# Kernel tuning notes

Hardware: AMD Instinct MI355X
Metric: run time of the kernel (lower is better)

## Reference

```python
import jax, jax.numpy as jnp
import numpy as np

N = 50000      # nodes
E = 800000     # edges (avg degree 16)
D = 128        # in_dim
H = 128        # hidden_dim
C = 10         # num_classes
G = 128        # graphs in batch
NUM_LAYERS = 3


def setup_inputs() -> dict:
    key = jax.random.key(0)
    ks = jax.random.split(key, 32)
    inp = {
        'features': jax.random.normal(ks[0], (N, D), dtype=jnp.float32),
        'src': jax.random.randint(ks[1], (E,), 0, N, dtype=jnp.int32),
        'dst': jax.random.randint(ks[2], (E,), 0, N, dtype=jnp.int32),
        'graph_ids': jnp.sort(jax.random.randint(ks[3], (N,), 0, G, dtype=jnp.int32)),
        'eps': jnp.zeros((NUM_LAYERS,), dtype=jnp.float32),  # learn_eps=True, init 0
    }
    # GIN MLPs: layer i has linear1 [in,H], linear2 [H,H] (stored as [in,out])
    ki = 4
    for i in range(NUM_LAYERS):
        din = D if i == 0 else H
        inp[f'w1_{i}'] = jax.random.normal(ks[ki], (din, H), dtype=jnp.float32) * (1.0 / np.sqrt(din)); ki += 1
        inp[f'b1_{i}'] = jnp.zeros((H,), dtype=jnp.float32)
        inp[f'w2_{i}'] = jax.random.normal(ks[ki], (H, H), dtype=jnp.float32) * (1.0 / np.sqrt(H)); ki += 1
        inp[f'b2_{i}'] = jnp.zeros((H,), dtype=jnp.float32)
    inp['wc1'] = jax.random.normal(ks[ki], (H, H), dtype=jnp.float32) * (1.0 / np.sqrt(H)); ki += 1
    inp['bc1'] = jnp.zeros((H,), dtype=jnp.float32)
    inp['wc2'] = jax.random.normal(ks[ki], (H, C), dtype=jnp.float32) * (1.0 / np.sqrt(H)); ki += 1
    inp['bc2'] = jnp.zeros((C,), dtype=jnp.float32)
    return inp


def _mlp(x, w1, b1, w2, b2):
    return jax.nn.relu(x @ w1 + b1) @ w2 + b2


def reference(features, src, dst, graph_ids, eps,
              w1_0, b1_0, w2_0, b2_0,
              w1_1, b1_1, w2_1, b2_1,
              w1_2, b1_2, w2_2, b2_2,
              wc1, bc1, wc2, bc2):
    mlps = [(w1_0, b1_0, w2_0, b2_0), (w1_1, b1_1, w2_1, b2_1), (w1_2, b1_2, w2_2, b2_2)]
    h = features
    for i, (w1, b1, w2, b2) in enumerate(mlps):
        # GINConv: aggregate sum of in-neighbor features (gather src, segment-sum into dst)
        agg = jax.ops.segment_sum(h[src], dst, num_segments=N)
        h = (1.0 + eps[i]) * h + agg
        h = _mlp(h, w1, b1, w2, b2)
        h = jax.nn.relu(h)
    # SumPooling: nodes -> graphs
    hg = jax.ops.segment_sum(h, graph_ids, num_segments=G)  # [G, H]
    out = jax.nn.relu(hg @ wc1 + bc1) @ wc2 + bc2            # [G, C]
    return out
```

## Files before the change

kernel.cpp:

```cpp
#include <hip/hip_runtime.h>

#define NN 50000
#define EE 800000
#define HH 128
#define CC 10
#define GG 128
#define NBK 782
#define NCH 98
#define CHUNK 8192

typedef __attribute__((ext_vector_type(8))) short short8;
typedef __attribute__((ext_vector_type(4))) float f32x4;

__device__ __forceinline__ ushort f2b(float f) {
    union { float f; uint u; } x; x.f = f;
    uint u = x.u;
    uint r = (u + 0x7fffu + ((u >> 16) & 1u)) >> 16;
    return (ushort)r;
}
__device__ __forceinline__ float lo2f(uint v) {
    union { uint u; float f; } x; x.u = v << 16; return x.f;
}
__device__ __forceinline__ float hi2f(uint v) {
    union { uint u; float f; } x; x.u = v & 0xffff0000u; return x.f;
}


__global__ __launch_bounds__(256) void hist_kernel(const int* __restrict__ dst,
                                                   int* __restrict__ hist) {
    __shared__ int hc[NBK];
    const int c = blockIdx.x, t = threadIdx.x;
    for (int k = t; k < NBK; k += 256) hc[k] = 0;
    __syncthreads();
    for (int j = 0; j < 32; ++j) {
        int e = c * CHUNK + j * 256 + t;
        if (e < EE) atomicAdd(&hc[dst[e] >> 6], 1);
    }
    __syncthreads();
    for (int k = t; k < NBK; k += 256) hist[k * NCH + c] = hc[k];
}

__global__ __launch_bounds__(128) void bscan_kernel(const int* __restrict__ hist,
                                                    int* __restrict__ rel,
                                                    int* __restrict__ btot) {
    __shared__ int s[128];
    const int b = blockIdx.x, t = threadIdx.x;
    int v = (t < NCH) ? hist[b * NCH + t] : 0;
    s[t] = v;
    __syncthreads();
    for (int off = 1; off < 128; off <<= 1) {
        int tt = (t >= off) ? s[t - off] : 0;
        __syncthreads();
        s[t] += tt;
        __syncthreads();
    }
    if (t < NCH) rel[b * NCH + t] = s[t] - v;
    if (t == 127) btot[b] = s[127];
}

__global__ __launch_bounds__(1024) void tscan_kernel(const int* __restrict__ btot,
                                                     int* __restrict__ bucketptr,
                                                     int* __restrict__ rowptr) {
    __shared__ int s[1024];
    const int t = threadIdx.x;
    int v = (t < NBK) ? btot[t] : 0;
    s[t] = v;
    __syncthreads();
    for (int off = 1; off < 1024; off <<= 1) {
        int tt = (t >= off) ? s[t - off] : 0;
        __syncthreads();
        s[t] += tt;
        __syncthreads();
    }
    if (t < NBK) bucketptr[t] = s[t] - v;
    if (t == 0) { bucketptr[NBK] = EE; rowptr[NN] = EE; }
}

__global__ __launch_bounds__(256) void scatter_kernel(const int* __restrict__ src,
                                                      const int* __restrict__ dst,
                                                      const int* __restrict__ rel,
                                                      const int* __restrict__ bucketptr,
                                                      int* __restrict__ epk) {
    __shared__ int cur[NBK];
    const int c = blockIdx.x, t = threadIdx.x;
    for (int k = t; k < NBK; k += 256) cur[k] = bucketptr[k] + rel[k * NCH + c];
    __syncthreads();
    for (int j = 0; j < 32; ++j) {
        int e = c * CHUNK + j * 256 + t;
        if (e < EE) {
            int d = dst[e];
            int bk = d >> 6;
            int pos = atomicAdd(&cur[bk], 1);
            epk[pos] = ((d & 63) << 16) | src[e];
        }
    }
}

__global__ __launch_bounds__(256) void bsort_kernel(const int* __restrict__ epk,
                                                    const int* __restrict__ bucketptr,
                                                    int* __restrict__ eidx,
                                                    int* __restrict__ rowptr) {
    __shared__ int cnt[64];
    __shared__ int cur[64];
    const int b = blockIdx.x, t = threadIdx.x;
    const int base = bucketptr[b], end = bucketptr[b + 1];
    if (t < 64) cnt[t] = 0;
    __syncthreads();
    for (int i = base + t; i < end; i += 256)
        atomicAdd(&cnt[(epk[i] >> 16) & 63], 1);
    __syncthreads();
    if (t < 64) {
        int v = cnt[t];
        int incl = v;
#pragma unroll
        for (int off = 1; off < 64; off <<= 1) {
            int u = __shfl_up(incl, off);
            if (t >= off) incl += u;
        }
        int excl = incl - v;
        cur[t] = excl;
        int node = b * 64 + t;
        if (node < NN) rowptr[node] = base + excl;
    }
    __syncthreads();
    for (int i = base + t; i < end; i += 256) {
        int p = epk[i];
        int dl = (p >> 16) & 63;
        int pos = atomicAdd(&cur[dl], 1);
        eidx[base + pos] = p & 0xffff;
    }
}


__global__ __launch_bounds__(256) void f2b_kernel(const float* __restrict__ in,
                                                  ushort* __restrict__ out, int n4) {
    int i = blockIdx.x * 256 + threadIdx.x;
    if (i < n4) {
        float4 v = ((const float4*)in)[i];
        ushort4 o;
        o.x = f2b(v.x); o.y = f2b(v.y); o.z = f2b(v.z); o.w = f2b(v.w);
        ((ushort4*)out)[i] = o;
    }
}

__global__ __launch_bounds__(256) void wconv_kernel(const float* w0, const float* w1,
                                                    const float* w2, const float* w3,
                                                    const float* w4, const float* w5,
                                                    ushort* __restrict__ wt) {
    const float* src;
    switch (blockIdx.y) {
        case 0: src = w0; break; case 1: src = w1; break;
        case 2: src = w2; break; case 3: src = w3; break;
        case 4: src = w4; break; default: src = w5; break;
    }
    int idx = blockIdx.x * 256 + threadIdx.x;
    int n = idx >> 7, k = idx & 127;
    wt[blockIdx.y * 16384 + n * 128 + k] = f2b(src[k * 128 + n]);
}


__global__ __launch_bounds__(256) void aggregate_kernel(const ushort* __restrict__ h,
                                                        const int* __restrict__ rowptr,
                                                        const int* __restrict__ eidx,
                                                        const float* __restrict__ epsp,
                                                        int layer,
                                                        ushort* __restrict__ xb) {
    int node = blockIdx.x * 4 + (threadIdx.x >> 6);
    if (node >= NN) return;
    int lane = threadIdx.x & 63;
    int half = lane >> 5, li = lane & 31;
    int beg = rowptr[node], end = rowptr[node + 1];
    float c0 = 0.f, c1 = 0.f, c2 = 0.f, c3 = 0.f;
    int i = beg + half;
    for (; i + 6 < end; i += 8) {
        int s0 = eidx[i], s1 = eidx[i + 2], s2 = eidx[i + 4], s3 = eidx[i + 6];
        uint2 v0 = *(const uint2*)(h + (size_t)s0 * HH + li * 4);
        uint2 v1 = *(const uint2*)(h + (size_t)s1 * HH + li * 4);
        uint2 v2 = *(const uint2*)(h + (size_t)s2 * HH + li * 4);
        uint2 v3 = *(const uint2*)(h + (size_t)s3 * HH + li * 4);
        c0 += lo2f(v0.x) + lo2f(v1.x) + lo2f(v2.x) + lo2f(v3.x);
        c1 += hi2f(v0.x) + hi2f(v1.x) + hi2f(v2.x) + hi2f(v3.x);
        c2 += lo2f(v0.y) + lo2f(v1.y) + lo2f(v2.y) + lo2f(v3.y);
        c3 += hi2f(v0.y) + hi2f(v1.y) + hi2f(v2.y) + hi2f(v3.y);
    }
    for (; i < end; i += 2) {
        int s0 = eidx[i];
        uint2 v0 = *(const uint2*)(h + (size_t)s0 * HH + li * 4);
        c0 += lo2f(v0.x); c1 += hi2f(v0.x);
        c2 += lo2f(v0.y); c3 += hi2f(v0.y);
    }
    c0 += __shfl_xor(c0, 32);
    c1 += __shfl_xor(c1, 32);
    c2 += __shfl_xor(c2, 32);
    c3 += __shfl_xor(c3, 32);
    if (half == 0) {
        uint2 hv = *(const uint2*)(h + (size_t)node * HH + li * 4);
        float e = 1.0f + epsp[layer];
        ushort4 o;
        o.x = f2b(e * lo2f(hv.x) + c0);
        o.y = f2b(e * hi2f(hv.x) + c1);
        o.z = f2b(e * lo2f(hv.y) + c2);
        o.w = f2b(e * hi2f(hv.y) + c3);
        *(ushort4*)(xb + (size_t)node * HH + li * 4) = o;
    }
}


template <bool LAST>
__global__ __launch_bounds__(256) void fused_mlp(const ushort* __restrict__ xb,
                                                 const ushort* __restrict__ wt1,
                                                 const ushort* __restrict__ wt2,
                                                 const float* __restrict__ b1,
                                                 const float* __restrict__ b2,
                                                 const int* __restrict__ gid,
                                                 float* __restrict__ hg,
                                                 ushort* __restrict__ out, int nrows) {
    __shared__ __align__(16) ushort xs[64][136];
    __shared__ __align__(16) ushort hs[64][136];
    const int tid = threadIdx.x;
    const int lane = tid & 63, w = tid >> 6;
    const int row0 = blockIdx.x * 64;
    const int l15 = lane & 15, lhi = lane >> 4;

    short8 a1[2][4], a2[2][4];
#pragma unroll
    for (int fa = 0; fa < 2; ++fa)
#pragma unroll
        for (int kt = 0; kt < 4; ++kt) {
            int n = w * 32 + fa * 16 + l15;
            int k = kt * 32 + lhi * 8;
            a1[fa][kt] = *(const short8*)(wt1 + n * HH + k);
            a2[fa][kt] = *(const short8*)(wt2 + n * HH + k);
        }

#pragma unroll
    for (int it = 0; it < 4; ++it) {
        int idx = it * 256 + tid;
        int r = idx >> 4, kq = idx & 15;
        int row = row0 + r;
        uint4 xv = make_uint4(0u, 0u, 0u, 0u);
        if (row < nrows) xv = *(const uint4*)(xb + (size_t)row * HH + kq * 8);
        *(uint4*)&xs[r][kq * 8] = xv;
    }
    __syncthreads();

    f32x4 acc[2][4];
#pragma unroll
    for (int fa = 0; fa < 2; ++fa)
#pragma unroll
        for (int fb = 0; fb < 4; ++fb) acc[fa][fb] = (f32x4)(0.f);
#pragma unroll
    for (int kt = 0; kt < 4; ++kt) {
        short8 bfr[4];
#pragma unroll
        for (int fb = 0; fb < 4; ++fb)
            bfr[fb] = *(const short8*)&xs[fb * 16 + l15][kt * 32 + lhi * 8];
#pragma unroll
        for (int fa = 0; fa < 2; ++fa)
#pragma unroll
            for (int fb = 0; fb < 4; ++fb)
                acc[fa][fb] = __builtin_amdgcn_mfma_f32_16x16x32_bf16(a1[fa][kt], bfr[fb],
                                                                     acc[fa][fb], 0, 0, 0);
    }

#pragma unroll
    for (int fa = 0; fa < 2; ++fa) {
        int nb = w * 32 + fa * 16 + lhi * 4;
        float4 bv = *(const float4*)(b1 + nb);
#pragma unroll
        for (int fb = 0; fb < 4; ++fb) {
            ushort4 o;
            o.x = f2b(fmaxf(acc[fa][fb][0] + bv.x, 0.f));
            o.y = f2b(fmaxf(acc[fa][fb][1] + bv.y, 0.f));
            o.z = f2b(fmaxf(acc[fa][fb][2] + bv.z, 0.f));
            o.w = f2b(fmaxf(acc[fa][fb][3] + bv.w, 0.f));
            *(ushort4*)&hs[fb * 16 + l15][nb] = o;
        }
    }
    __syncthreads();

#pragma unroll
    for (int fa = 0; fa < 2; ++fa)
#pragma unroll
        for (int fb = 0; fb < 4; ++fb) acc[fa][fb] = (f32x4)(0.f);
#pragma unroll
    for (int kt = 0; kt < 4; ++kt) {
        short8 bfr[4];
#pragma unroll
        for (int fb = 0; fb < 4; ++fb)
            bfr[fb] = *(const short8*)&hs[fb * 16 + l15][kt * 32 + lhi * 8];
#pragma unroll
        for (int fa = 0; fa < 2; ++fa)
#pragma unroll
            for (int fb = 0; fb < 4; ++fb)
                acc[fa][fb] = __builtin_amdgcn_mfma_f32_16x16x32_bf16(a2[fa][kt], bfr[fb],
                                                                     acc[fa][fb], 0, 0, 0);
    }

#pragma unroll
    for (int fa = 0; fa < 2; ++fa) {
        int nb = w * 32 + fa * 16 + lhi * 4;
        float4 bv = *(const float4*)(b2 + nb);
#pragma unroll
        for (int fb = 0; fb < 4; ++fb) {
            int m = row0 + fb * 16 + l15;
            ushort4 o;
            o.x = f2b(fmaxf(acc[fa][fb][0] + bv.x, 0.f));
            o.y = f2b(fmaxf(acc[fa][fb][1] + bv.y, 0.f));
            o.z = f2b(fmaxf(acc[fa][fb][2] + bv.z, 0.f));
            o.w = f2b(fmaxf(acc[fa][fb][3] + bv.w, 0.f));
            if (LAST) {
                *(ushort4*)&xs[fb * 16 + l15][nb] = o;
            } else if (m < nrows) {
                *(ushort4*)(out + (size_t)m * HH + nb) = o;
            }
        }
    }

    if (LAST) {
        __syncthreads();
        int j = tid & 63;
        int rg = tid >> 6;
        float ax = 0.f, ay = 0.f;
        int gcur = -1;
#pragma unroll
        for (int ii = 0; ii < 16; ++ii) {
            int r = rg + ii * 4;
            int n = row0 + r;
            if (n >= nrows) break;
            int g = gid[n];
            if (g != gcur) {
                if (gcur >= 0) {
                    atomicAdd(&hg[gcur * HH + 2 * j], ax);
                    atomicAdd(&hg[gcur * HH + 2 * j + 1], ay);
                }
                gcur = g; ax = 0.f; ay = 0.f;
            }
            uint v = *(const uint*)&xs[r][2 * j];
            ax += lo2f(v); ay += hi2f(v);
        }
        if (gcur >= 0) {
            atomicAdd(&hg[gcur * HH + 2 * j], ax);
            atomicAdd(&hg[gcur * HH + 2 * j + 1], ay);
        }
    }
}


__global__ __launch_bounds__(128) void classify_kernel(const float* __restrict__ hg,
                                                       const float* __restrict__ wc1,
                                                       const float* __restrict__ bc1,
                                                       const float* __restrict__ wc2,
                                                       const float* __restrict__ bc2,
                                                       float* __restrict__ out) {
    __shared__ float xrow[HH];
    __shared__ float trow[HH];
    int g = blockIdx.x, j = threadIdx.x;
    xrow[j] = hg[g * HH + j];
    __syncthreads();
    float s = bc1[j];
#pragma unroll 8
    for (int k = 0; k < HH; ++k) s += xrow[k] * wc1[k * HH + j];
    trow[j] = fmaxf(s, 0.f);
    __syncthreads();
    if (j < CC) {
        float o = bc2[j];
#pragma unroll 8
        for (int k = 0; k < HH; ++k) o += trow[k] * wc2[k * CC + j];
        out[g * CC + j] = o;
    }
}

extern "C" void kernel_launch(void* const* d_in, const int* in_sizes, int n_in,
                              void* d_out, int out_size, void* d_ws, size_t ws_size,
                              hipStream_t stream) {
    const float* features = (const float*)d_in[0];
    const int* src = (const int*)d_in[1];
    const int* dst = (const int*)d_in[2];
    const int* gid = (const int*)d_in[3];
    const float* eps = (const float*)d_in[4];
    const float* w1[3] = {(const float*)d_in[5], (const float*)d_in[9], (const float*)d_in[13]};
    const float* b1[3] = {(const float*)d_in[6], (const float*)d_in[10], (const float*)d_in[14]};
    const float* w2[3] = {(const float*)d_in[7], (const float*)d_in[11], (const float*)d_in[15]};
    const float* b2[3] = {(const float*)d_in[8], (const float*)d_in[12], (const float*)d_in[16]};
    const float* wc1 = (const float*)d_in[17];
    const float* bc1 = (const float*)d_in[18];
    const float* wc2 = (const float*)d_in[19];
    const float* bc2 = (const float*)d_in[20];
    float* outp = (float*)d_out;

    char* ws = (char*)d_ws;
    size_t off = 0;
    auto alloc = [&](size_t bytes) {
        void* p = ws + off;
        off += (bytes + 255) & ~(size_t)255;
        return p;
    };
    int* hist = (int*)alloc((size_t)NBK * NCH * sizeof(int));
    int* rel = (int*)alloc((size_t)NBK * NCH * sizeof(int));
    int* btot = (int*)alloc(NBK * sizeof(int));
    int* bucketptr = (int*)alloc((NBK + 1) * sizeof(int));
    int* epk = (int*)alloc(EE * sizeof(int));
    int* eidx = (int*)alloc(EE * sizeof(int));
    int* rowptr = (int*)alloc((NN + 1) * sizeof(int));
    ushort* hb0 = (ushort*)alloc((size_t)NN * HH * 2);
    ushort* hbuf = (ushort*)alloc((size_t)NN * HH * 2);
    ushort* xb = (ushort*)alloc((size_t)NN * HH * 2);
    ushort* wtb = (ushort*)alloc(6 * 16384 * 2);
    float* hg = (float*)alloc(GG * HH * sizeof(float));

    hist_kernel<<<NCH, 256, 0, stream>>>(dst, hist);
    bscan_kernel<<<NBK, 128, 0, stream>>>(hist, rel, btot);
    tscan_kernel<<<1, 1024, 0, stream>>>(btot, bucketptr, rowptr);
    scatter_kernel<<<NCH, 256, 0, stream>>>(src, dst, rel, bucketptr, epk);
    bsort_kernel<<<NBK, 256, 0, stream>>>(epk, bucketptr, eidx, rowptr);

    f2b_kernel<<<(NN * HH / 4 + 255) / 256, 256, 0, stream>>>(features, hb0, NN * HH / 4);
    dim3 wg(64, 6);
    wconv_kernel<<<wg, 256, 0, stream>>>(w1[0], w2[0], w1[1], w2[1], w1[2], w2[2], wtb);

    hipMemsetAsync(hg, 0, GG * HH * sizeof(float), stream);

    const int GB = (NN + 63) / 64;
    const int AB = (NN + 3) / 4;

    aggregate_kernel<<<AB, 256, 0, stream>>>(hb0, rowptr, eidx, eps, 0, xb);
    fused_mlp<false><<<GB, 256, 0, stream>>>(xb, wtb + 0 * 16384, wtb + 1 * 16384,
                                             b1[0], b2[0], gid, hg, hbuf, NN);
    aggregate_kernel<<<AB, 256, 0, stream>>>(hbuf, rowptr, eidx, eps, 1, xb);
    fused_mlp<false><<<GB, 256, 0, stream>>>(xb, wtb + 2 * 16384, wtb + 3 * 16384,
                                             b1[1], b2[1], gid, hg, hbuf, NN);
    aggregate_kernel<<<AB, 256, 0, stream>>>(hbuf, rowptr, eidx, eps, 2, xb);
    fused_mlp<true><<<GB, 256, 0, stream>>>(xb, wtb + 4 * 16384, wtb + 5 * 16384,
                                            b1[2], b2[2], gid, hg, nullptr, NN);

    classify_kernel<<<GG, 128, 0, stream>>>(hg, wc1, bc1, wc2, bc2, outp);
}
```

Baseline: 233.3 us.

## Store node features in 32-column planes and shrink edge indices to ushort

Node feature buffers move from row-major [N,128] to four planes of [N,32] bf16. The aggregate kernel is split into 4 slices, each gathering 64-byte rows from one plane, with 16 lanes per node and 8 loads kept in flight. The goal is to shrink the gathered working set per pass so it fits in cache better. Edge source indices are stored as ushort, which is incorrect for node ids of 65536 or more but fine for N=50000. The f2b, weight-conversion and histogram kernels are merged into one prep launch to cut launch overhead.

```diff
diff --git a/kernel.cpp b/kernel.cpp
--- a/kernel.cpp
+++ b/kernel.cpp
@@ -8,6 +8,7 @@
 #define NBK 782
 #define NCH 98
 #define CHUNK 8192
+#define PL (NN * 32)
 
 typedef __attribute__((ext_vector_type(8))) short short8;
 typedef __attribute__((ext_vector_type(4))) float f32x4;
@@ -26,18 +27,46 @@
 }
 
 
-__global__ __launch_bounds__(256) void hist_kernel(const int* __restrict__ dst,
+__global__ __launch_bounds__(256) void prep_kernel(const float* __restrict__ features,
+                                                   const float* w0, const float* w1,
+                                                   const float* w2, const float* w3,
+                                                   const float* w4, const float* w5,
+                                                   const int* __restrict__ dst,
+                                                   ushort* __restrict__ hb0,
+                                                   ushort* __restrict__ wt,
                                                    int* __restrict__ hist) {
     __shared__ int hc[NBK];
-    const int c = blockIdx.x, t = threadIdx.x;
-    for (int k = t; k < NBK; k += 256) hc[k] = 0;
-    __syncthreads();
-    for (int j = 0; j < 32; ++j) {
-        int e = c * CHUNK + j * 256 + t;
-        if (e < EE) atomicAdd(&hc[dst[e] >> 6], 1);
-    }
-    __syncthreads();
-    for (int k = t; k < NBK; k += 256) hist[k * NCH + c] = hc[k];
+    const int b = blockIdx.x, t = threadIdx.x;
+    if (b < 6250) {
+        int idx = b * 256 + t;
+        int n = idx >> 5, j = idx & 31;
+        float4 v = *(const float4*)(features + (size_t)n * HH + j * 4);
+        ushort4 o;
+        o.x = f2b(v.x); o.y = f2b(v.y); o.z = f2b(v.z); o.w = f2b(v.w);
+        int plane = j >> 3;
+        *(ushort4*)(hb0 + (size_t)plane * PL + (size_t)n * 32 + (j & 7) * 4) = o;
+    } else if (b < 6634) {
+        int idx = (b - 6250) * 256 + t;
+        int mi = idx >> 14, rest = idx & 16383;
+        int n = rest >> 7, k = rest & 127;
+        const float* src;
+        switch (mi) {
+            case 0: src = w0; break; case 1: src = w1; break;
+            case 2: src = w2; break; case 3: src = w3; break;
+            case 4: src = w4; break; default: src = w5; break;
+        }
+        wt[mi * 16384 + n * 128 + k] = f2b(src[k * 128 + n]);
+    } else {
+        const int c = b - 6634;
+        for (int k = t; k < NBK; k += 256) hc[k] = 0;
+        __syncthreads();
+        for (int j = 0; j < 32; ++j) {
+            int e = c * CHUNK + j * 256 + t;
+            if (e < EE) atomicAdd(&hc[dst[e] >> 6], 1);
+        }
+        __syncthreads();
+        for (int k = t; k < NBK; k += 256) hist[k * NCH + c] = hc[k];
+    }
 }
 
 __global__ __launch_bounds__(128) void bscan_kernel(const int* __restrict__ hist,
@@ -98,7 +127,7 @@
 
 __global__ __launch_bounds__(256) void bsort_kernel(const int* __restrict__ epk,
                                                     const int* __restrict__ bucketptr,
-                                                    int* __restrict__ eidx,
+                                                    ushort* __restrict__ eidx,
                                                     int* __restrict__ rowptr) {
     __shared__ int cnt[64];
     __shared__ int cur[64];
@@ -127,82 +156,46 @@
         int p = epk[i];
         int dl = (p >> 16) & 63;
         int pos = atomicAdd(&cur[dl], 1);
-        eidx[base + pos] = p & 0xffff;
-    }
-}
-
-
-__global__ __launch_bounds__(256) void f2b_kernel(const float* __restrict__ in,
-                                                  ushort* __restrict__ out, int n4) {
-    int i = blockIdx.x * 256 + threadIdx.x;
-    if (i < n4) {
-        float4 v = ((const float4*)in)[i];
-        ushort4 o;
-        o.x = f2b(v.x); o.y = f2b(v.y); o.z = f2b(v.z); o.w = f2b(v.w);
-        ((ushort4*)out)[i] = o;
-    }
-}
-
-__global__ __launch_bounds__(256) void wconv_kernel(const float* w0, const float* w1,
-                                                    const float* w2, const float* w3,
-                                                    const float* w4, const float* w5,
-                                                    ushort* __restrict__ wt) {
-    const float* src;
-    switch (blockIdx.y) {
-        case 0: src = w0; break; case 1: src = w1; break;
-        case 2: src = w2; break; case 3: src = w3; break;
-        case 4: src = w4; break; default: src = w5; break;
-    }
-    int idx = blockIdx.x * 256 + threadIdx.x;
-    int n = idx >> 7, k = idx & 127;
-    wt[blockIdx.y * 16384 + n * 128 + k] = f2b(src[k * 128 + n]);
+        eidx[base + pos] = (ushort)(p & 0xffff);
+    }
 }
 
 
 __global__ __launch_bounds__(256) void aggregate_kernel(const ushort* __restrict__ h,
                                                         const int* __restrict__ rowptr,
-                                                        const int* __restrict__ eidx,
+                                                        const ushort* __restrict__ eidx,
                                                         const float* __restrict__ epsp,
                                                         int layer,
                                                         ushort* __restrict__ xb) {
-    int node = blockIdx.x * 4 + (threadIdx.x >> 6);
-    if (node >= NN) return;
-    int lane = threadIdx.x & 63;
-    int half = lane >> 5, li = lane & 31;
-    int beg = rowptr[node], end = rowptr[node + 1];
-    float c0 = 0.f, c1 = 0.f, c2 = 0.f, c3 = 0.f;
-    int i = beg + half;
-    for (; i + 6 < end; i += 8) {
-        int s0 = eidx[i], s1 = eidx[i + 2], s2 = eidx[i + 4], s3 = eidx[i + 6];
-        uint2 v0 = *(const uint2*)(h + (size_t)s0 * HH + li * 4);
-        uint2 v1 = *(const uint2*)(h + (size_t)s1 * HH + li * 4);
-        uint2 v2 = *(const uint2*)(h + (size_t)s2 * HH + li * 4);
-        uint2 v3 = *(const uint2*)(h + (size_t)s3 * HH + li * 4);
-        c0 += lo2f(v0.x) + lo2f(v1.x) + lo2f(v2.x) + lo2f(v3.x);
-        c1 += hi2f(v0.x) + hi2f(v1.x) + hi2f(v2.x) + hi2f(v3.x);
-        c2 += lo2f(v0.y) + lo2f(v1.y) + lo2f(v2.y) + lo2f(v3.y);
-        c3 += hi2f(v0.y) + hi2f(v1.y) + hi2f(v2.y) + hi2f(v3.y);
-    }
-    for (; i < end; i += 2) {
-        int s0 = eidx[i];
-        uint2 v0 = *(const uint2*)(h + (size_t)s0 * HH + li * 4);
-        c0 += lo2f(v0.x); c1 += hi2f(v0.x);
-        c2 += lo2f(v0.y); c3 += hi2f(v0.y);
-    }
-    c0 += __shfl_xor(c0, 32);
-    c1 += __shfl_xor(c1, 32);
-    c2 += __shfl_xor(c2, 32);
-    c3 += __shfl_xor(c3, 32);
-    if (half == 0) {
-        uint2 hv = *(const uint2*)(h + (size_t)node * HH + li * 4);
-        float e = 1.0f + epsp[layer];
-        ushort4 o;
-        o.x = f2b(e * lo2f(hv.x) + c0);
-        o.y = f2b(e * hi2f(hv.x) + c1);
-        o.z = f2b(e * lo2f(hv.y) + c2);
-        o.w = f2b(e * hi2f(hv.y) + c3);
-        *(ushort4*)(xb + (size_t)node * HH + li * 4) = o;
-    }
+    const int bid = blockIdx.x;
+    const int slice = bid / 3125;
+    const int grp = bid % 3125;
+    const int w = threadIdx.x >> 6, l = threadIdx.x & 63;
+    const int q = l >> 4, lq = l & 15;
+    const int node = grp * 16 + w * 4 + q;
+    const ushort* hp = h + (size_t)slice * PL;
+    const int beg = rowptr[node], end = rowptr[node + 1];
+    float c0 = 0.f, c1 = 0.f;
+    int i = beg;
+    for (; i + 8 <= end; i += 8) {
+        int s[8];
+        uint v[8];
+#pragma unroll
+        for (int k = 0; k < 8; ++k) s[k] = eidx[i + k];
+#pragma unroll
+        for (int k = 0; k < 8; ++k) v[k] = *(const uint*)(hp + (size_t)s[k] * 32 + lq * 2);
+#pragma unroll
+        for (int k = 0; k < 8; ++k) { c0 += lo2f(v[k]); c1 += hi2f(v[k]); }
+    }
+    for (; i < end; ++i) {
+        int s = eidx[i];
+        uint v = *(const uint*)(hp + (size_t)s * 32 + lq * 2);
+        c0 += lo2f(v); c1 += hi2f(v);
+    }
+    uint hv = *(const uint*)(hp + (size_t)node * 32 + lq * 2);
+    float e = 1.0f + epsp[layer];
+    uint o = (uint)f2b(e * lo2f(hv) + c0) | (((uint)f2b(e * hi2f(hv) + c1)) << 16);
+    *(uint*)(xb + (size_t)slice * PL + (size_t)node * 32 + lq * 2) = o;
 }
 
 
@@ -214,7 +207,8 @@
                                                  const float* __restrict__ b2,
                                                  const int* __restrict__ gid,
                                                  float* __restrict__ hg,
-                                                 ushort* __restrict__ out, int nrows) {
+                                                 ushort* __restrict__ out,
+                                                 int nrows) {
     __shared__ __align__(16) ushort xs[64][136];
     __shared__ __align__(16) ushort hs[64][136];
     const int tid = threadIdx.x;
@@ -239,7 +233,8 @@
         int r = idx >> 4, kq = idx & 15;
         int row = row0 + r;
         uint4 xv = make_uint4(0u, 0u, 0u, 0u);
-        if (row < nrows) xv = *(const uint4*)(xb + (size_t)row * HH + kq * 8);
+        if (row < nrows)
+            xv = *(const uint4*)(xb + (size_t)(kq >> 2) * PL + (size_t)row * 32 + (kq & 3) * 8);
         *(uint4*)&xs[r][kq * 8] = xv;
     }
     __syncthreads();
@@ -312,7 +307,7 @@
             if (LAST) {
                 *(ushort4*)&xs[fb * 16 + l15][nb] = o;
             } else if (m < nrows) {
-                *(ushort4*)(out + (size_t)m * HH + nb) = o;
+                *(ushort4*)(out + (size_t)(nb >> 5) * PL + (size_t)m * 32 + (nb & 31)) = o;
             }
         }
     }
@@ -401,7 +396,7 @@
     int* btot = (int*)alloc(NBK * sizeof(int));
     int* bucketptr = (int*)alloc((NBK + 1) * sizeof(int));
     int* epk = (int*)alloc(EE * sizeof(int));
-    int* eidx = (int*)alloc(EE * sizeof(int));
+    ushort* eidx = (ushort*)alloc(EE * sizeof(ushort));
     int* rowptr = (int*)alloc((NN + 1) * sizeof(int));
     ushort* hb0 = (ushort*)alloc((size_t)NN * HH * 2);
     ushort* hbuf = (ushort*)alloc((size_t)NN * HH * 2);
@@ -409,20 +404,17 @@
     ushort* wtb = (ushort*)alloc(6 * 16384 * 2);
     float* hg = (float*)alloc(GG * HH * sizeof(float));
 
-    hist_kernel<<<NCH, 256, 0, stream>>>(dst, hist);
+    prep_kernel<<<6732, 256, 0, stream>>>(features, w1[0], w2[0], w1[1], w2[1], w1[2], w2[2],
+                                          dst, hb0, wtb, hist);
     bscan_kernel<<<NBK, 128, 0, stream>>>(hist, rel, btot);
     tscan_kernel<<<1, 1024, 0, stream>>>(btot, bucketptr, rowptr);
     scatter_kernel<<<NCH, 256, 0, stream>>>(src, dst, rel, bucketptr, epk);
     bsort_kernel<<<NBK, 256, 0, stream>>>(epk, bucketptr, eidx, rowptr);
 
-    f2b_kernel<<<(NN * HH / 4 + 255) / 256, 256, 0, stream>>>(features, hb0, NN * HH / 4);
-    dim3 wg(64, 6);
-    wconv_kernel<<<wg, 256, 0, stream>>>(w1[0], w2[0], w1[1], w2[1], w1[2], w2[2], wtb);
-
     hipMemsetAsync(hg, 0, GG * HH * sizeof(float), stream);
 
     const int GB = (NN + 63) / 64;
-    const int AB = (NN + 3) / 4;
+    const int AB = 12500;
 
     aggregate_kernel<<<AB, 256, 0, stream>>>(hb0, rowptr, eidx, eps, 0, xb);
     fused_mlp<false><<<GB, 256, 0, stream>>>(xb, wtb + 0 * 16384, wtb + 1 * 16384,
```

New measurement: 259.3 us. 1.11x slower.
